# Kernel tuning notes

Measured on AMD Instinct MI355X. Metric: run time of the kernel, lower is better.

The kernel has to match this reference:

```python
import jax, jax.numpy as jnp
import numpy as np

B, G, S = 8, 64, 256
DIM = 41           # input_dim = enc_in*2+1
ET = 128           # embed_time = d_model+1
H = 8              # num_heads
EK = ET // H       # per-head time-embed dim
NH = 127           # nhidden = d_model


def setup_inputs() -> dict:
    key = jax.random.key(0)
    ks = jax.random.split(key, 12)
    inp = {
        "query": jax.random.normal(ks[0], (B, G, ET), jnp.float32),
        "key": jax.random.normal(ks[1], (B, S, DIM), jnp.float32),
        "value": jax.random.normal(ks[2], (B, S, DIM), jnp.float32),
        "mask": jax.random.randint(ks[3], (B, S, DIM), 0, 2).astype(jnp.float32),
        "qt": jnp.linspace(0.0, 1.0, G, dtype=jnp.float32),
        "tt": jax.random.uniform(ks[4], (B, S), jnp.float32),
        "stride_in": jnp.zeros((DIM,), jnp.float32),
        # learned params (torch Linear convention: y = x @ W.T + b; we store W already transposed)
        "Wq": jax.random.normal(ks[5], (ET, ET), jnp.float32) / np.sqrt(ET),
        "bq": jnp.zeros((ET,), jnp.float32),
        "Wk": jax.random.normal(ks[6], (DIM, ET), jnp.float32) / np.sqrt(DIM),
        "bk": jnp.zeros((ET,), jnp.float32),
        "Wo": jax.random.normal(ks[7], (DIM * H, NH), jnp.float32) / np.sqrt(DIM * H),
        "bo": jnp.zeros((NH,), jnp.float32),
        "Wr": jax.random.normal(ks[8], (DIM, DIM), jnp.float32) / np.sqrt(DIM),
        "br": jnp.zeros((DIM,), jnp.float32),
    }
    return inp


def reference(query, key, value, mask, qt, tt, stride_in, Wq, bq, Wk, bk, Wo, bo, Wr, br):
    b, s, dim = value.shape
    # per-head projections of time embeddings
    q = (query @ Wq + bq).reshape(b, -1, H, EK).transpose(0, 2, 1, 3)   # [B,H,G,EK]
    k = (key @ Wk + bk).reshape(b, -1, H, EK).transpose(0, 2, 1, 3)     # [B,H,S,EK]
    # per-channel time window half-width: sigmoid(range(stride_list))
    stride = jax.nn.sigmoid(stride_in @ Wr + br)                        # [DIM]
    # time-window mask m[b,g,s,d] = (tt in [qt[g]-stride[d], qt[g]+stride[d]]) & observed
    lo = qt[:, None] - stride[None, :]                                  # [G,DIM]
    hi = qt[:, None] + stride[None, :]                                  # [G,DIM]
    ttd = tt[:, None, :, None]                                          # [B,1,S,1]
    m = (ttd <= hi[None, :, None, :]) & (ttd >= lo[None, :, None, :])   # [B,G,S,DIM]
    m = m & (mask[:, None, :, :] != 0)
    # scaled dot-product scores, broadcast over value dim with per-dim masking
    scores = jnp.einsum('bhge,bhse->bhgs', q, k) / jnp.sqrt(jnp.float32(EK))
    scores = jnp.where(m[:, None], scores[..., None], jnp.float32(-1e9))  # [B,H,G,S,DIM]
    p_attn = jax.nn.softmax(scores, axis=-2)                              # softmax over S
    x = jnp.einsum('bhgsd,bsd->bhgd', p_attn, value)                      # [B,H,G,DIM]
    x = x.transpose(0, 2, 1, 3).reshape(b, -1, H * dim)                   # [B,G,H*DIM]
    out = x @ Wo + bo                                                     # [B,G,NH]
    return out
```

## Files before the change

kernel.cpp:

```cpp
#include <hip/hip_runtime.h>
#include <math.h>

#define B 8
#define G 64
#define S 256
#define DIM 41
#define ET 128
#define H 8
#define EK 16
#define NH 127
#define HD (H*DIM)
#define EROW 257

__global__ __launch_bounds__(256) void prep_kernel(const float* __restrict__ key,
                                                   const float* __restrict__ Wk,
                                                   const float* __restrict__ bk,
                                                   const float* __restrict__ query,
                                                   const float* __restrict__ Wq,
                                                   const float* __restrict__ bq,
                                                   const float* __restrict__ mask,
                                                   const float* __restrict__ qt,
                                                   const float* __restrict__ tt,
                                                   const float* __restrict__ stride_in,
                                                   const float* __restrict__ Wr,
                                                   const float* __restrict__ br,
                                                   float* __restrict__ kpT,
                                                   float* __restrict__ qp,
                                                   unsigned int* __restrict__ embitsT) {
    __shared__ float smem[5248 + 64];
    const int bid = blockIdx.x;
    const int tid = threadIdx.x;

    if (bid < 1024) {
        float* k0 = smem;
        float* k1 = smem + 48;
        const int half = tid >> 7;
        const int j = tid & 127;
        const int row = bid * 2 + half;
        if (j < DIM) (half ? k1 : k0)[j] = key[row * DIM + j];
        __syncthreads();
        const float* kr = half ? k1 : k0;
        float acc = bk[j];
#pragma unroll
        for (int i = 0; i < DIM; ++i) acc = fmaf(kr[i], Wk[i * ET + j], acc);
        const int b = row >> 8, s = row & 255;
        kpT[b * 32768 + (j >> 2) * 1024 + s * 4 + (j & 3)] = acc;
    } else if (bid < 1280) {
        float* qlds = smem;
        const int base = (bid - 1024) * 2;
        qlds[tid] = query[base * ET + tid];
        __syncthreads();
        const int half = tid >> 7;
        const int j = tid & 127;
        const float* qr = qlds + half * 128;
        float a0 = 0.f, a1 = 0.f, a2 = 0.f, a3 = 0.f;
#pragma unroll 8
        for (int i = 0; i < ET; i += 4) {
            a0 = fmaf(qr[i + 0], Wq[(i + 0) * ET + j], a0);
            a1 = fmaf(qr[i + 1], Wq[(i + 1) * ET + j], a1);
            a2 = fmaf(qr[i + 2], Wq[(i + 2) * ET + j], a2);
            a3 = fmaf(qr[i + 3], Wq[(i + 3) * ET + j], a3);
        }
        qp[(base + half) * ET + j] = bq[j] + ((a0 + a1) + (a2 + a3));
    } else {
        float* mlds = smem;
        float* strd = smem + 5248;
        const int bg = bid - 1280;
        const int b = bg >> 6, g = bg & 63;
        if (tid < DIM) {
            float a = br[tid];
            for (int i = 0; i < DIM; ++i) a = fmaf(stride_in[i], Wr[i * DIM + tid], a);
            strd[tid] = 1.0f / (1.0f + expf(-a));
        }
        __syncthreads();
        const float qtg = qt[g];
        for (int rr = 0; rr < 2; ++rr) {
            for (int idx = tid; idx < 5248; idx += 256)
                mlds[idx] = mask[(size_t)b * S * DIM + rr * 5248 + idx];
            __syncthreads();
            if (tid < 128) {
                const int s = rr * 128 + tid;
                const float t = tt[b * S + s];
                const int wv = tid >> 6;
                const int w = rr * 2 + wv;
                unsigned int* op = embitsT + (size_t)bg * (DIM * 8) + w * 2;
#pragma unroll
                for (int d = 0; d < DIM; ++d) {
                    const float sd = strd[d];
                    const int ok = (t >= qtg - sd) & (t <= qtg + sd) & (mlds[tid * DIM + d] != 0.0f);
                    const unsigned long long bal = __ballot(ok);
                    if ((tid & 63) == 0) {
                        op[d * 8 + 0] = (unsigned int)bal;
                        op[d * 8 + 1] = (unsigned int)(bal >> 32);
                    }
                }
            }
            __syncthreads();
        }
    }
}

__global__ __launch_bounds__(256) void attn_kernel(const float* __restrict__ kpT,
                                                   const float* __restrict__ qp,
                                                   const unsigned int* __restrict__ embitsT,
                                                   const float* __restrict__ value,
                                                   float* __restrict__ x) {
    __shared__ float elds[4 * EROW];
    __shared__ float qlds[64];
    __shared__ float Mb[4];

    const int bid = blockIdx.x;
    const int bg = bid >> 1;
    const int hq = bid & 1;
    const int b = bg >> 6;
    const int tid = threadIdx.x;

    if (tid < 64) qlds[tid] = qp[(size_t)bg * ET + hq * 64 + tid];
    __syncthreads();

    float sc4[4];
    {
        const int s = tid;
        const float4* kb = reinterpret_cast<const float4*>(kpT) + (size_t)b * 8192 + s;
#pragma unroll
        for (int hl = 0; hl < 4; ++hl) {
            const int h = hq * 4 + hl;
            float a = 0.f;
#pragma unroll
            for (int e4 = 0; e4 < 4; ++e4) {
                const float4 kv = kb[(h * 4 + e4) * 256];
                a = fmaf(qlds[hl * EK + e4 * 4 + 0], kv.x, a);
                a = fmaf(qlds[hl * EK + e4 * 4 + 1], kv.y, a);
                a = fmaf(qlds[hl * EK + e4 * 4 + 2], kv.z, a);
                a = fmaf(qlds[hl * EK + e4 * 4 + 3], kv.w, a);
            }
            sc4[hl] = a * 0.25f;
            elds[hl * EROW + s] = sc4[hl];
        }
    }
    __syncthreads();

    if (tid < 128) {
        const int hl = tid >> 5, j = tid & 31;
        float m = elds[hl * EROW + j];
#pragma unroll
        for (int k = 1; k < 8; ++k) m = fmaxf(m, elds[hl * EROW + j + 32 * k]);
#pragma unroll
        for (int off = 16; off; off >>= 1) m = fmaxf(m, __shfl_xor(m, off, 32));
        if (j == 0) Mb[hl] = m;
    }
    __syncthreads();

    {
        const int s = tid;
#pragma unroll
        for (int hl = 0; hl < 4; ++hl) elds[hl * EROW + s] = __expf(sc4[hl] - Mb[hl]);
    }
    __syncthreads();

    {
        const int w = tid >> 6;
        const int d = tid & 63;
        if (d < DIM) {
            const uint4* bp = reinterpret_cast<const uint4*>(embitsT + (size_t)bg * (DIM * 8) + d * 8);
            const uint4 b0 = bp[0], b1 = bp[1];
            const unsigned int bw[8] = {b0.x, b0.y, b0.z, b0.w, b1.x, b1.y, b1.z, b1.w};
            const float* er = &elds[w * EROW];
            const float* vb = value + (size_t)b * S * DIM + d;
            float Ssum = 0.f, acc = 0.f;
#pragma unroll
            for (int k = 0; k < 8; ++k) {
                const unsigned int wv = bw[k];
#pragma unroll 8
                for (int i = 0; i < 32; ++i) {
                    const int s = k * 32 + i;
                    const float e = er[s];
                    const float v = vb[(size_t)s * DIM];
                    const float wgt = ((wv >> i) & 1u) ? e : 0.f;
                    Ssum += wgt;
                    acc = fmaf(wgt, v, acc);
                }
            }
            float r;
            if (Ssum != 0.f) {
                r = acc / Ssum;
            } else {
                float vs = 0.f;
                for (int s2 = 0; s2 < S; ++s2) vs += vb[(size_t)s2 * DIM];
                r = vs * (1.0f / S);
            }
            x[(size_t)bg * HD + (hq * 4 + w) * DIM + d] = r;
        }
    }
}

__global__ __launch_bounds__(128) void outproj_kernel(const float* __restrict__ x,
                                                      const float* __restrict__ Wo,
                                                      const float* __restrict__ bo,
                                                      float* __restrict__ out) {
    __shared__ float xr[HD];
    const int bg = blockIdx.x;
    const int tid = threadIdx.x;
    xr[tid] = x[(size_t)bg * HD + tid];
    xr[tid + 128] = x[(size_t)bg * HD + tid + 128];
    if (tid < HD - 256) xr[tid + 256] = x[(size_t)bg * HD + tid + 256];
    __syncthreads();
    if (tid < NH) {
        const int n = tid;
        float a0 = 0.f, a1 = 0.f, a2 = 0.f, a3 = 0.f;
#pragma unroll 2
        for (int i = 0; i < HD; i += 4) {
            a0 = fmaf(xr[i + 0], Wo[(size_t)(i + 0) * NH + n], a0);
            a1 = fmaf(xr[i + 1], Wo[(size_t)(i + 1) * NH + n], a1);
            a2 = fmaf(xr[i + 2], Wo[(size_t)(i + 2) * NH + n], a2);
            a3 = fmaf(xr[i + 3], Wo[(size_t)(i + 3) * NH + n], a3);
        }
        out[(size_t)bg * NH + n] = bo[n] + ((a0 + a1) + (a2 + a3));
    }
}

extern "C" void kernel_launch(void* const* d_in, const int* in_sizes, int n_in,
                              void* d_out, int out_size, void* d_ws, size_t ws_size,
                              hipStream_t stream) {
    const float* query     = (const float*)d_in[0];
    const float* key       = (const float*)d_in[1];
    const float* value     = (const float*)d_in[2];
    const float* mask      = (const float*)d_in[3];
    const float* qt        = (const float*)d_in[4];
    const float* tt        = (const float*)d_in[5];
    const float* stride_in = (const float*)d_in[6];
    const float* Wq        = (const float*)d_in[7];
    const float* bq        = (const float*)d_in[8];
    const float* Wk        = (const float*)d_in[9];
    const float* bk        = (const float*)d_in[10];
    const float* Wo        = (const float*)d_in[11];
    const float* bo        = (const float*)d_in[12];
    const float* Wr        = (const float*)d_in[13];
    const float* br        = (const float*)d_in[14];
    float* out = (float*)d_out;

    float* kpT = (float*)d_ws;
    float* qp = kpT + (size_t)B * H * 4 * S * 4;
    unsigned int* embitsT = (unsigned int*)(qp + (size_t)B * G * ET);
    float* x = (float*)(embitsT + (size_t)B * G * DIM * 8);

    prep_kernel<<<1792, 256, 0, stream>>>(key, Wk, bk, query, Wq, bq, mask, qt, tt,
                                          stride_in, Wr, br, kpT, qp, embitsT);
    attn_kernel<<<B * G * 2, 256, 0, stream>>>(kpT, qp, embitsT, value, x);
    outproj_kernel<<<B * G, 128, 0, stream>>>(x, Wo, bo, out);
}
```

Measured before the change: 39.91 us.

## Fuse output projection into attention kernel with atomic accumulation

Removes the separate output-projection kernel and the intermediate x buffer. Each attention block now multiplies its four heads' results by the matching slice of Wo, split across two thread halves and combined in shared memory. The two blocks per (b,g) then atomically add their partial sums into out, which is zeroed first with a memset. This saves one kernel launch and a global round-trip, but adds a memset, atomics, and a non-deterministic summation order.

```diff
diff --git a/kernel.cpp b/kernel.cpp
--- a/kernel.cpp
+++ b/kernel.cpp
@@ -104,10 +104,14 @@
                                                    const float* __restrict__ qp,
                                                    const unsigned int* __restrict__ embitsT,
                                                    const float* __restrict__ value,
-                                                   float* __restrict__ x) {
+                                                   const float* __restrict__ Wo,
+                                                   const float* __restrict__ bo,
+                                                   float* __restrict__ out) {
     __shared__ float elds[4 * EROW];
     __shared__ float qlds[64];
     __shared__ float Mb[4];
+    __shared__ float xq[4 * DIM];
+    __shared__ float po[2][128];
 
     const int bid = blockIdx.x;
     const int bg = bid >> 1;
@@ -189,33 +193,29 @@
                 for (int s2 = 0; s2 < S; ++s2) vs += vb[(size_t)s2 * DIM];
                 r = vs * (1.0f / S);
             }
-            x[(size_t)bg * HD + (hq * 4 + w) * DIM + d] = r;
-        }
-    }
-}
-
-__global__ __launch_bounds__(128) void outproj_kernel(const float* __restrict__ x,
-                                                      const float* __restrict__ Wo,
-                                                      const float* __restrict__ bo,
-                                                      float* __restrict__ out) {
-    __shared__ float xr[HD];
-    const int bg = blockIdx.x;
-    const int tid = threadIdx.x;
-    xr[tid] = x[(size_t)bg * HD + tid];
-    xr[tid + 128] = x[(size_t)bg * HD + tid + 128];
-    if (tid < HD - 256) xr[tid + 256] = x[(size_t)bg * HD + tid + 256];
+            xq[w * DIM + d] = r;
+        }
+    }
+    __syncthreads();
+
+    {
+        const int n = tid & 127, c = tid >> 7;
+        if (n < NH) {
+            const int i0 = c * 82;
+            float a0 = 0.f, a1 = 0.f;
+#pragma unroll 2
+            for (int i = i0; i < i0 + 82; i += 2) {
+                a0 = fmaf(xq[i],     Wo[(size_t)(hq * 164 + i) * NH + n],     a0);
+                a1 = fmaf(xq[i + 1], Wo[(size_t)(hq * 164 + i + 1) * NH + n], a1);
+            }
+            po[c][n] = a0 + a1;
+        }
+    }
     __syncthreads();
     if (tid < NH) {
-        const int n = tid;
-        float a0 = 0.f, a1 = 0.f, a2 = 0.f, a3 = 0.f;
-#pragma unroll 2
-        for (int i = 0; i < HD; i += 4) {
-            a0 = fmaf(xr[i + 0], Wo[(size_t)(i + 0) * NH + n], a0);
-            a1 = fmaf(xr[i + 1], Wo[(size_t)(i + 1) * NH + n], a1);
-            a2 = fmaf(xr[i + 2], Wo[(size_t)(i + 2) * NH + n], a2);
-            a3 = fmaf(xr[i + 3], Wo[(size_t)(i + 3) * NH + n], a3);
-        }
-        out[(size_t)bg * NH + n] = bo[n] + ((a0 + a1) + (a2 + a3));
+        float val = po[0][tid] + po[1][tid];
+        if (hq == 0) val += bo[tid];
+        atomicAdd(&out[(size_t)bg * NH + tid], val);
     }
 }
 
@@ -242,10 +242,10 @@
     float* kpT = (float*)d_ws;
     float* qp = kpT + (size_t)B * H * 4 * S * 4;
     unsigned int* embitsT = (unsigned int*)(qp + (size_t)B * G * ET);
-    float* x = (float*)(embitsT + (size_t)B * G * DIM * 8);
+
+    hipMemsetAsync(out, 0, (size_t)out_size * sizeof(float), stream);
 
     prep_kernel<<<1792, 256, 0, stream>>>(key, Wk, bk, query, Wq, bq, mask, qt, tt,
                                           stride_in, Wr, br, kpT, qp, embitsT);
-    attn_kernel<<<B * G * 2, 256, 0, stream>>>(kpT, qp, embitsT, value, x);
-    outproj_kernel<<<B * G, 128, 0, stream>>>(x, Wo, bo, out);
+    attn_kernel<<<B * G * 2, 256, 0, stream>>>(kpT, qp, embitsT, value, Wo, bo, out);
 }
```

After: 43.86 us. 9.9% more time.
